# Optimization experiments

Measured on AMD Instinct MI355X. Metric: run time of the kernel, lower is better.

Reference implementation:

```python
import jax, jax.numpy as jnp
import numpy as np

B, L, S, LA, NA, E, D, H, NHID = 16, 256, 100, 48, 32, 64, 768, 12, 1024
W_IDX = S + 2
EPS = 1e-12


def setup_inputs() -> dict:
    rng = np.random.default_rng(0)
    key = jax.random.key(0)
    ks = jax.random.split(key, 8)
    idxs = np.zeros((B, W_IDX), dtype=np.int64)
    bert_lens = np.zeros((B,), dtype=np.int64)
    is_trig = np.zeros((B, S), dtype=np.float32)
    ent_map = np.zeros((B, S, E), dtype=np.float32)
    argw_mask = np.zeros((B, LA, 1), dtype=np.float32)
    for b in range(B):
        sb = int(rng.integers(60, S + 1))          # n first-subword tokens
        ab = int(rng.integers(8, LA + 1))          # n arg-role subwords
        sent_idx = np.sort(rng.choice(np.arange(1, 2 * sb + 1), size=sb, replace=False))
        sls = 2 * sb + 1                           # second-to-last [SEP] position
        last = sls + ab + 1                        # last [SEP] position
        idxs[b, :sb] = sent_idx
        idxs[b, sb] = sls
        idxs[b, sb + 1] = last
        bert_lens[b] = last + 1
        t0 = int(rng.integers(0, sb - 1))
        is_trig[b, t0:t0 + 2] = 1.0
        eb = int(rng.integers(16, E + 1))
        for e in range(eb):
            ent_map[b, int(rng.integers(0, sb)), e] = 1.0
        argw_mask[b, :ab, 0] = 1.0
    arg_w = np.asarray(jax.random.uniform(ks[0], (B, LA, NA), dtype=jnp.float32)) * argw_mask
    return {
        'all_embeddings': jax.random.normal(ks[1], (B, L, D), dtype=jnp.float32),
        'is_triggers': jnp.asarray(is_trig),
        'arg_weight_matrices': jnp.asarray(arg_w, dtype=jnp.float32),
        'entity_mapping': jnp.asarray(ent_map),
        'att0': jax.random.uniform(ks[2], (B, H, L, L), dtype=jnp.float32),
        'att1': jax.random.uniform(ks[3], (B, H, L, L), dtype=jnp.float32),
        'att2': jax.random.uniform(ks[4], (B, H, L, L), dtype=jnp.float32),
        'W_ta': jax.random.normal(ks[5], (3 * D, D), dtype=jnp.float32) * 0.02,
        'b_ta': jnp.zeros((D,), dtype=jnp.float32),
        'W1': jax.random.normal(ks[6], (6 * D, NHID), dtype=jnp.float32) * 0.02,
        'b1': jnp.zeros((NHID,), dtype=jnp.float32),
        'W2': jax.random.normal(ks[7], (NHID, 1), dtype=jnp.float32) * 0.02,
        'b2': jnp.zeros((1,), dtype=jnp.float32),
        'idxs_to_collect': jnp.asarray(idxs),
        'bert_sentence_lengths': jnp.asarray(bert_lens),
    }


def _l1_normalize(x, axis):
    # F.normalize(x, p=1, dim=axis)
    return x / jnp.clip(jnp.sum(jnp.abs(x), axis=axis, keepdims=True), EPS)


def reference(all_embeddings, is_triggers, arg_weight_matrices, entity_mapping,
              att0, att1, att2, W_ta, b_ta, W1, b1, W2, b2,
              idxs_to_collect, bert_sentence_lengths):
    idxs = idxs_to_collect
    valid = idxs > 0                                   # [B,W]
    n_valid = jnp.sum(valid, axis=1)                   # [B]
    j = jnp.arange(S)
    sent_valid = (j[None, :] < (n_valid - 2)[:, None]).astype(all_embeddings.dtype)  # [B,S]
    sent_idx = idxs[:, :S]
    # first-subword gather, zero-padded (get_fist_subword_embeddings)
    sent_emb = jnp.take_along_axis(all_embeddings, sent_idx[:, :, None], axis=1) * sent_valid[:, :, None]
    # arg-role segment: (second_last_sep+1) .. (bert_len-2), zero-padded to LA
    sls = jnp.take_along_axis(idxs, (n_valid - 2)[:, None], axis=1)[:, 0]   # [B]
    arg_pos = sls[:, None] + 1 + jnp.arange(LA)[None, :]                    # [B,LA]
    arg_valid = (arg_pos < (bert_sentence_lengths - 1)[:, None]).astype(all_embeddings.dtype)
    arg_emb0 = jnp.take_along_axis(all_embeddings, jnp.clip(arg_pos, 0, L - 1)[:, :, None], axis=1) * arg_valid[:, :, None]
    # entity aggregation + trigger mean pooling
    entity = jnp.einsum('bsd,bse->bed', sent_emb, entity_mapping)           # [B,E,D]
    trig = jnp.sum(sent_emb * is_triggers[:, :, None], axis=1) / jnp.sum(is_triggers, axis=1)[:, None]
    arg = jnp.einsum('bld,bla->bad', arg_emb0, arg_weight_matrices)         # [B,NA,D]
    # trigger-aware entity fusion
    trig_e = jnp.broadcast_to(trig[:, None, :], entity.shape)
    nonempty = (jnp.sum(jnp.abs(entity), axis=-1) > 0).astype(entity.dtype)
    ent_cat = jnp.concatenate([entity, trig_e, entity * trig_e], axis=-1)   # [B,E,3D]
    entity = (ent_cat @ W_ta + b_ta) * nonempty[:, :, None]
    # bidirectional token<->arg attention (L1-normalized)
    score = jnp.einsum('bed,bad->bea', entity, arg) / np.sqrt(D)            # [B,E,NA]
    t2a = _l1_normalize(score, 2)[..., None]
    a2t = _l1_normalize(score, 1)[..., None]
    token_argAwared = jnp.sum(arg[:, None] * t2a, axis=2)                   # [B,E,D]
    arg_tokenAwared = jnp.sum(entity[:, :, None] * a2t, axis=1)             # [B,NA,D]
    # select_hidden_att: head-mean, gather collected rows/cols, row-renormalize
    def sel_att(att):
        m = jnp.mean(att, axis=1)                                           # [B,L,L]
        r = jnp.take_along_axis(m, sent_idx[:, :, None], axis=1)            # [B,S,L]
        c = jnp.take_along_axis(r, sent_idx[:, None, :], axis=2)            # [B,S,S]
        c = c * sent_valid[:, :, None] * sent_valid[:, None, :]
        return c / jnp.clip(jnp.sum(c, axis=-1, keepdims=True), EPS)
    t2t = (sel_att(att0) + sel_att(att1) + sel_att(att2)) / 3.0             # [B,S,S]
    a_h2h_tok = t2t @ sent_emb                                              # [B,S,D]
    A_h2h = jnp.einsum('bse,bsd->bed', entity_mapping, a_h2h_tok)           # [B,E,D]
    H_ = jnp.einsum('bse,bsd->bed', entity_mapping, sent_emb)               # [B,E,D]
    a2a = jax.nn.softmax(arg @ jnp.swapaxes(arg, -1, -2), axis=-1)
    A_u2u = a2a @ arg                                                       # [B,NA,D]
    shp = (B, E, NA, D)
    latent = jnp.concatenate([
        jnp.broadcast_to(H_[:, :, None], shp),
        jnp.broadcast_to(arg[:, None], shp),
        jnp.broadcast_to(token_argAwared[:, :, None], shp),
        jnp.broadcast_to(A_h2h[:, :, None], shp),
        jnp.broadcast_to(arg_tokenAwared[:, None], shp),
        jnp.broadcast_to(A_u2u[:, None], shp),
    ], axis=-1)                                                             # [B,E,NA,6D]
    h = jax.nn.gelu(latent @ W1 + b1, approximate=False)
    out = (h @ W2 + b2)[..., 0]                                             # [B,E,NA]
    return out
```

## Files before the change

kernel.cpp:

```cpp
#include <hip/hip_runtime.h>
#include <math.h>

#define B_ 16
#define L_ 256
#define S_ 100
#define LA_ 48
#define NA_ 32
#define E_ 64
#define D_ 768
#define H_ 12
#define NHID_ 1024
#define WIDX_ 102
#define EPSF 1e-12f

typedef __attribute__((ext_vector_type(8))) short s16x8;
typedef __attribute__((ext_vector_type(4))) float f32x4;

__device__ __forceinline__ void split_bf16(float x, unsigned short& h, unsigned short& l) {
  unsigned u = __float_as_uint(x);
  unsigned hr = u + 0x7FFFu + ((u >> 16) & 1u);
  h = (unsigned short)(hr >> 16);
  float r = x - __uint_as_float(hr & 0xFFFF0000u);
  unsigned u2 = __float_as_uint(r);
  unsigned lr = u2 + 0x7FFFu + ((u2 >> 16) & 1u);
  l = (unsigned short)(lr >> 16);
}

__global__ void k_meta(const int* __restrict__ idxs, const int* __restrict__ blen,
                       int* __restrict__ meta) {
  int b = blockIdx.x, t = threadIdx.x;
  __shared__ int cnt;
  if (t == 0) cnt = 0;
  __syncthreads();
  if (t < WIDX_ && idxs[b * WIDX_ + t] > 0) atomicAdd(&cnt, 1);
  __syncthreads();
  if (t == 0) {
    int sb = cnt - 2;
    meta[b * 4 + 0] = sb;
    meta[b * 4 + 1] = idxs[b * WIDX_ + sb];
    meta[b * 4 + 2] = blen[b] - 1;
  }
}

__global__ void k_gather(const float* __restrict__ emb, const int* __restrict__ idxs,
                         const int* __restrict__ meta, float* __restrict__ sent_emb,
                         float* __restrict__ arg_emb) {
  int b = blockIdx.y, y = blockIdx.x, t = threadIdx.x;
  int sb = meta[b * 4 + 0], sls = meta[b * 4 + 1], last = meta[b * 4 + 2];
  if (y < S_) {
    int s = y;
    float* dst = sent_emb + ((size_t)b * S_ + s) * D_;
    if (s < sb) {
      const float* src = emb + ((size_t)b * L_ + idxs[b * WIDX_ + s]) * D_;
      for (int d = t; d < D_; d += 256) dst[d] = src[d];
    } else {
      for (int d = t; d < D_; d += 256) dst[d] = 0.f;
    }
  } else {
    int l = y - S_;
    int pos = sls + 1 + l;
    float* dst = arg_emb + ((size_t)b * LA_ + l) * D_;
    if (pos < last) {
      int p = pos > (L_ - 1) ? (L_ - 1) : pos;
      const float* src = emb + ((size_t)b * L_ + p) * D_;
      for (int d = t; d < D_; d += 256) dst[d] = src[d];
    } else {
      for (int d = t; d < D_; d += 256) dst[d] = 0.f;
    }
  }
}

__global__ void k_trig(const float* __restrict__ sent_emb, const float* __restrict__ is_trig,
                       float* __restrict__ trig) {
  int b = blockIdx.y;
  int d = blockIdx.x * 256 + threadIdx.x;
  float acc = 0.f, den = 0.f;
  for (int s = 0; s < S_; s++) {
    float w = is_trig[b * S_ + s];
    den += w;
    if (w != 0.f) acc += w * sent_emb[((size_t)b * S_ + s) * D_ + d];
  }
  trig[b * D_ + d] = acc / den;
}

__global__ __launch_bounds__(256) void k_entity0(const float* __restrict__ sent_emb,
                                                 const float* __restrict__ ent_map,
                                                 const float* __restrict__ trig,
                                                 unsigned short* __restrict__ e0h,
                                                 unsigned short* __restrict__ e0l,
                                                 unsigned short* __restrict__ e0th,
                                                 unsigned short* __restrict__ e0tl,
                                                 float* __restrict__ ne) {
  int b = blockIdx.y, e = blockIdx.x, t = threadIdx.x;
  float a0 = 0.f, a1 = 0.f, a2 = 0.f;
  for (int s = 0; s < S_; s++) {
    float w = ent_map[((size_t)b * S_ + s) * E_ + e];
    if (w != 0.f) {
      const float* r = sent_emb + ((size_t)b * S_ + s) * D_;
      a0 += w * r[t]; a1 += w * r[t + 256]; a2 += w * r[t + 512];
    }
  }
  size_t o = ((size_t)b * E_ + e) * D_;
  const float* tr = trig + b * D_;
  unsigned short h, lo;
  split_bf16(a0, h, lo); e0h[o + t] = h; e0l[o + t] = lo;
  split_bf16(a1, h, lo); e0h[o + t + 256] = h; e0l[o + t + 256] = lo;
  split_bf16(a2, h, lo); e0h[o + t + 512] = h; e0l[o + t + 512] = lo;
  split_bf16(a0 * tr[t], h, lo); e0th[o + t] = h; e0tl[o + t] = lo;
  split_bf16(a1 * tr[t + 256], h, lo); e0th[o + t + 256] = h; e0tl[o + t + 256] = lo;
  split_bf16(a2 * tr[t + 512], h, lo); e0th[o + t + 512] = h; e0tl[o + t + 512] = lo;
  __shared__ float red[256];
  red[t] = fabsf(a0) + fabsf(a1) + fabsf(a2);
  __syncthreads();
  for (int s2 = 128; s2 > 0; s2 >>= 1) {
    if (t < s2) red[t] += red[t + s2];
    __syncthreads();
  }
  if (t == 0) ne[b * E_ + e] = (red[0] > 0.f) ? 1.f : 0.f;
}

__global__ __launch_bounds__(256) void k_wsum(const float* __restrict__ Wm, int wstride, int sy,
                                              int sx, const float* __restrict__ Vm,
                                              float* __restrict__ Om,
                                              unsigned short* __restrict__ oh,
                                              unsigned short* __restrict__ ol, int Y) {
  int b = blockIdx.y, x = blockIdx.x, t = threadIdx.x;
  float a0 = 0.f, a1 = 0.f, a2 = 0.f;
  const float* wb = Wm + (size_t)b * wstride + (size_t)x * sx;
  const float* vb = Vm + (size_t)b * Y * D_;
  for (int y = 0; y < Y; y++) {
    float w = wb[(size_t)y * sy];
    if (w != 0.f) {
      const float* r = vb + (size_t)y * D_;
      a0 += w * r[t]; a1 += w * r[t + 256]; a2 += w * r[t + 512];
    }
  }
  size_t oidx = ((size_t)b * gridDim.x + x) * D_;
  if (Om) {
    Om[oidx + t] = a0; Om[oidx + t + 256] = a1; Om[oidx + t + 512] = a2;
  }
  if (oh) {
    unsigned short h, lo;
    split_bf16(a0, h, lo); oh[oidx + t] = h; ol[oidx + t] = lo;
    split_bf16(a1, h, lo); oh[oidx + t + 256] = h; ol[oidx + t + 256] = lo;
    split_bf16(a2, h, lo); oh[oidx + t + 512] = h; ol[oidx + t + 512] = lo;
  }
}

__global__ void k_tb(const float* __restrict__ trig, const float* __restrict__ W_ta,
                     const float* __restrict__ b_ta, float* __restrict__ tb) {
  int b = blockIdx.y;
  int d = blockIdx.x * 256 + threadIdx.x;
  float acc0 = b_ta[d], acc1 = 0.f, acc2 = 0.f, acc3 = 0.f;
  float acc4 = 0.f, acc5 = 0.f, acc6 = 0.f, acc7 = 0.f;
  const float* tr = trig + b * D_;
  const float* w = W_ta + (size_t)D_ * D_ + d;
  for (int k = 0; k < D_; k += 8) {
    acc0 += tr[k + 0] * w[(size_t)(k + 0) * D_];
    acc1 += tr[k + 1] * w[(size_t)(k + 1) * D_];
    acc2 += tr[k + 2] * w[(size_t)(k + 2) * D_];
    acc3 += tr[k + 3] * w[(size_t)(k + 3) * D_];
    acc4 += tr[k + 4] * w[(size_t)(k + 4) * D_];
    acc5 += tr[k + 5] * w[(size_t)(k + 5) * D_];
    acc6 += tr[k + 6] * w[(size_t)(k + 6) * D_];
    acc7 += tr[k + 7] * w[(size_t)(k + 7) * D_];
  }
  tb[b * D_ + d] = ((acc0 + acc1) + (acc2 + acc3)) + ((acc4 + acc5) + (acc6 + acc7));
}

__global__ __launch_bounds__(256) void k_cvtT(const float* __restrict__ src, int K, int N,
                                              unsigned short* __restrict__ th,
                                              unsigned short* __restrict__ tl) {
  __shared__ float tile[32][33];
  int k0 = blockIdx.x * 32, n0 = blockIdx.y * 32;
  int tr = threadIdx.x >> 3, c4 = (threadIdx.x & 7) * 4;
  float4 v = *(const float4*)(src + (size_t)(k0 + tr) * N + n0 + c4);
  tile[tr][c4] = v.x; tile[tr][c4 + 1] = v.y; tile[tr][c4 + 2] = v.z; tile[tr][c4 + 3] = v.w;
  __syncthreads();
  unsigned short h[4], l[4];
#pragma unroll
  for (int i = 0; i < 4; ++i) split_bf16(tile[c4 + i][tr], h[i], l[i]);
  size_t oo = (size_t)(n0 + tr) * K + k0 + c4;
  th[oo + 0] = h[0]; th[oo + 1] = h[1]; th[oo + 2] = h[2]; th[oo + 3] = h[3];
  tl[oo + 0] = l[0]; tl[oo + 1] = l[1]; tl[oo + 2] = l[2]; tl[oo + 3] = l[3];
}

__global__ __launch_bounds__(256) void k_mgemm(
    int phase,
    const unsigned short* __restrict__ e0h, const unsigned short* __restrict__ e0l,
    const unsigned short* __restrict__ e0th, const unsigned short* __restrict__ e0tl,
    const unsigned short* __restrict__ Ah2hh, const unsigned short* __restrict__ Ah2hl,
    const unsigned short* __restrict__ argmh, const unsigned short* __restrict__ argml,
    const unsigned short* __restrict__ Au2uh, const unsigned short* __restrict__ Au2ul,
    const unsigned short* __restrict__ entnh, const unsigned short* __restrict__ entnl,
    const unsigned short* __restrict__ WtaTh, const unsigned short* __restrict__ WtaTl,
    const unsigned short* __restrict__ W1Th, const unsigned short* __restrict__ W1Tl,
    float* __restrict__ Cpe, float* __restrict__ PeAp, float* __restrict__ PaAp,
    float* __restrict__ P2p, float* __restrict__ Q2p) {
  int z = blockIdx.z;
  const unsigned short *Ah_, *Al_, *Bh_, *Bl_;
  float* C;
  int bstride, mtiles, niter, N, akoff, bkoff;
  const size_t HPE = (size_t)B_ * E_ * NHID_;
  const size_t HPA = (size_t)B_ * NA_ * NHID_;
  if (phase == 0) {
    int job = z >> 1, kh = z & 1;
    if (job == 0) {
      Ah_ = kh ? e0th : e0h; Al_ = kh ? e0tl : e0l; Bh_ = WtaTh; Bl_ = WtaTl;
      bstride = 2304; akoff = 0; bkoff = kh ? 1536 : 0;
      C = Cpe + (size_t)kh * 1024 * 768; N = 768; mtiles = 16; niter = 24;
    } else if (job == 1) {
      Ah_ = kh ? Ah2hh : e0h; Al_ = kh ? Ah2hl : e0l; Bh_ = W1Th; Bl_ = W1Tl;
      bstride = 4608; akoff = 0; bkoff = kh ? 3 * 768 : 0;
      C = PeAp + kh * HPE; N = 1024; mtiles = 16; niter = 24;
    } else if (job == 2) {
      Ah_ = kh ? Au2uh : argmh; Al_ = kh ? Au2ul : argml; Bh_ = W1Th; Bl_ = W1Tl;
      bstride = 4608; akoff = 0; bkoff = kh ? 5 * 768 : 768;
      C = PaAp + kh * HPA; N = 1024; mtiles = 8; niter = 24;
    } else {
      Ah_ = argmh; Al_ = argml; Bh_ = W1Th; Bl_ = W1Tl;
      bstride = 4608; akoff = kh * 384; bkoff = 2 * 768 + kh * 384;
      C = P2p + kh * HPA; N = 1024; mtiles = 8; niter = 12;
    }
  } else {
    int kh = z;
    Ah_ = entnh; Al_ = entnl; Bh_ = W1Th; Bl_ = W1Tl;
    bstride = 4608; akoff = kh * 384; bkoff = 4 * 768 + kh * 384;
    C = Q2p + kh * HPE; N = 1024; mtiles = 16; niter = 12;
  }
  int bx = blockIdx.x, by = blockIdx.y;
  if (by >= mtiles || bx * 64 >= N) return;

  __shared__ unsigned short As[2][2][64][4][8];
  __shared__ unsigned short Bs[2][2][64][4][8];

  int tid = threadIdx.x;
  int srow = tid >> 2, sg = tid & 3;
  int wc = sg ^ ((srow >> 1) & 3);
  const unsigned short* aPh = Ah_ + (size_t)(by * 64 + srow) * 768 + akoff + sg * 8;
  const unsigned short* aPl = Al_ + (size_t)(by * 64 + srow) * 768 + akoff + sg * 8;
  const unsigned short* bPh = Bh_ + (size_t)(bx * 64 + srow) * bstride + bkoff + sg * 8;
  const unsigned short* bPl = Bl_ + (size_t)(bx * 64 + srow) * bstride + bkoff + sg * 8;

  int lane = tid & 63, wave = tid >> 6;
  int wm = wave >> 1, wn = wave & 1;
  int fg = lane >> 4, fr = lane & 15;
  int ar0 = wm * 32 + fr;
  int bc0 = wn * 32 + fr;
  int ca = fg ^ ((ar0 >> 1) & 3);
  int cb = fg ^ ((bc0 >> 1) & 3);

  f32x4 acc00 = {0.f, 0.f, 0.f, 0.f}, acc01 = {0.f, 0.f, 0.f, 0.f};
  f32x4 acc10 = {0.f, 0.f, 0.f, 0.f}, acc11 = {0.f, 0.f, 0.f, 0.f};

  s16x8 a0h = *(const s16x8*)(aPh + 0), a0l = *(const s16x8*)(aPl + 0);
  s16x8 b0h = *(const s16x8*)(bPh + 0), b0l = *(const s16x8*)(bPl + 0);
  s16x8 a1h = *(const s16x8*)(aPh + 32), a1l = *(const s16x8*)(aPl + 32);
  s16x8 b1h = *(const s16x8*)(bPh + 32), b1l = *(const s16x8*)(bPl + 32);

#define WRITE_LDS(buf, ah, al, bh, bl)              \
  {                                                 \
    *(s16x8*)&As[buf][0][srow][wc][0] = ah;         \
    *(s16x8*)&As[buf][1][srow][wc][0] = al;         \
    *(s16x8*)&Bs[buf][0][srow][wc][0] = bh;         \
    *(s16x8*)&Bs[buf][1][srow][wc][0] = bl;         \
  }
#define LOAD_SET(ah, al, bh, bl, t_)                \
  {                                                 \
    ah = *(const s16x8*)(aPh + (t_) * 32);          \
    al = *(const s16x8*)(aPl + (t_) * 32);          \
    bh = *(const s16x8*)(bPh + (t_) * 32);          \
    bl = *(const s16x8*)(bPl + (t_) * 32);          \
  }
#define READ_MFMA(buf)                                                          \
  {                                                                             \
    s16x8 xah0 = *(const s16x8*)&As[buf][0][ar0][ca][0];                        \
    s16x8 xah1 = *(const s16x8*)&As[buf][0][ar0 + 16][ca][0];                   \
    s16x8 xal0 = *(const s16x8*)&As[buf][1][ar0][ca][0];                        \
    s16x8 xal1 = *(const s16x8*)&As[buf][1][ar0 + 16][ca][0];                   \
    s16x8 xbh0 = *(const s16x8*)&Bs[buf][0][bc0][cb][0];                        \
    s16x8 xbh1 = *(const s16x8*)&Bs[buf][0][bc0 + 16][cb][0];                   \
    s16x8 xbl0 = *(const s16x8*)&Bs[buf][1][bc0][cb][0];                        \
    s16x8 xbl1 = *(const s16x8*)&Bs[buf][1][bc0 + 16][cb][0];                   \
    acc00 = __builtin_amdgcn_mfma_f32_16x16x32_bf16(xah0, xbh0, acc00, 0, 0, 0); \
    acc00 = __builtin_amdgcn_mfma_f32_16x16x32_bf16(xah0, xbl0, acc00, 0, 0, 0); \
    acc00 = __builtin_amdgcn_mfma_f32_16x16x32_bf16(xal0, xbh0, acc00, 0, 0, 0); \
    acc01 = __builtin_amdgcn_mfma_f32_16x16x32_bf16(xah0, xbh1, acc01, 0, 0, 0); \
    acc01 = __builtin_amdgcn_mfma_f32_16x16x32_bf16(xah0, xbl1, acc01, 0, 0, 0); \
    acc01 = __builtin_amdgcn_mfma_f32_16x16x32_bf16(xal0, xbh1, acc01, 0, 0, 0); \
    acc10 = __builtin_amdgcn_mfma_f32_16x16x32_bf16(xah1, xbh0, acc10, 0, 0, 0); \
    acc10 = __builtin_amdgcn_mfma_f32_16x16x32_bf16(xah1, xbl0, acc10, 0, 0, 0); \
    acc10 = __builtin_amdgcn_mfma_f32_16x16x32_bf16(xal1, xbh0, acc10, 0, 0, 0); \
    acc11 = __builtin_amdgcn_mfma_f32_16x16x32_bf16(xah1, xbh1, acc11, 0, 0, 0); \
    acc11 = __builtin_amdgcn_mfma_f32_16x16x32_bf16(xah1, xbl1, acc11, 0, 0, 0); \
    acc11 = __builtin_amdgcn_mfma_f32_16x16x32_bf16(xal1, xbh1, acc11, 0, 0, 0); \
  }

  WRITE_LDS(0, a0h, a0l, b0h, b0l);
  LOAD_SET(a0h, a0l, b0h, b0l, 2);
  __syncthreads();

  for (int it = 0; it < niter; it += 2) {
    if (it + 1 < niter) {
      WRITE_LDS(1, a1h, a1l, b1h, b1l);
      if (it + 3 < niter) LOAD_SET(a1h, a1l, b1h, b1l, it + 3);
    }
    READ_MFMA(0);
    __syncthreads();
    if (it + 2 < niter) {
      WRITE_LDS(0, a0h, a0l, b0h, b0l);
      if (it + 4 < niter) LOAD_SET(a0h, a0l, b0h, b0l, it + 4);
    }
    READ_MFMA(1);
    __syncthreads();
  }
#undef WRITE_LDS
#undef LOAD_SET
#undef READ_MFMA

  f32x4 accs[2][2] = {{acc00, acc01}, {acc10, acc11}};
  int colb = bx * 64 + wn * 32 + fr;
  int rowb = by * 64 + wm * 32 + fg * 4;
#pragma unroll
  for (int i = 0; i < 2; ++i) {
#pragma unroll
    for (int j = 0; j < 2; ++j) {
      int col = colb + j * 16;
#pragma unroll
      for (int r = 0; r < 4; ++r) {
        int row = rowb + i * 16 + r;
        C[(size_t)row * N + col] = accs[i][j][r];
      }
    }
  }
}

__global__ __launch_bounds__(256) void k_combE(const float* __restrict__ Cpe,
                                               const float* __restrict__ tb,
                                               const float* __restrict__ ne,
                                               float* __restrict__ entn,
                                               unsigned short* __restrict__ entnh,
                                               unsigned short* __restrict__ entnl) {
  int t = threadIdx.x;
  int r0 = blockIdx.x * 4;
  const size_t HH = (size_t)1024 * 768;
#pragma unroll
  for (int i = 0; i < 4; ++i) {
    int row = r0 + i;
    int b = row >> 6;
    float nev = ne[row];
#pragma unroll
    for (int j = 0; j < 3; ++j) {
      int col = t + j * 256;
      size_t o = (size_t)row * D_ + col;
      float v = (Cpe[o] + Cpe[HH + o] + tb[(size_t)b * D_ + col]) * nev;
      entn[o] = v;
      unsigned short hh, ll;
      split_bf16(v, hh, ll);
      entnh[o] = hh; entnl[o] = ll;
    }
  }
}

__global__ __launch_bounds__(256) void k_score(const float* __restrict__ entn,
                                               const float* __restrict__ argm,
                                               float* __restrict__ score) {
  int b = blockIdx.y, e = blockIdx.x, t = threadIdx.x;
  __shared__ float ent[D_];
  const float* er = entn + ((size_t)b * E_ + e) * D_;
  for (int d = t; d < D_; d += 256) ent[d] = er[d];
  __syncthreads();
  int wave = t >> 6, lane = t & 63;
  const float scale = 0.03608439182435161f;
  for (int a = wave; a < NA_; a += 4) {
    const float* ar = argm + ((size_t)b * NA_ + a) * D_;
    float p = 0.f;
#pragma unroll
    for (int i = 0; i < 12; i++) {
      int d = lane + 64 * i;
      p += ent[d] * ar[d];
    }
    for (int off = 32; off > 0; off >>= 1) p += __shfl_down(p, off);
    if (lane == 0) score[((size_t)b * E_ + e) * NA_ + a] = p * scale;
  }
}

__global__ void k_norm(const float* __restrict__ score, float* __restrict__ t2a,
                       float* __restrict__ a2t) {
  int b = blockIdx.x, t = threadIdx.x;
  __shared__ float s[E_ * NA_];
  __shared__ float rs[E_];
  __shared__ float cs[NA_];
  for (int i = t; i < E_ * NA_; i += 256) s[i] = score[(size_t)b * E_ * NA_ + i];
  __syncthreads();
  if (t < E_) {
    float sum = 0.f;
    for (int a = 0; a < NA_; a++) sum += fabsf(s[t * NA_ + a]);
    rs[t] = fmaxf(sum, EPSF);
  } else if (t >= 64 && t < 96) {
    int a = t - 64;
    float sum = 0.f;
    for (int e = 0; e < E_; e++) sum += fabsf(s[e * NA_ + a]);
    cs[a] = fmaxf(sum, EPSF);
  }
  __syncthreads();
  for (int i = t; i < E_ * NA_; i += 256) {
    int e = i >> 5, a = i & 31;
    float v = s[i];
    t2a[(size_t)b * E_ * NA_ + i] = v / rs[e];
    a2t[(size_t)b * E_ * NA_ + i] = v / cs[a];
  }
}

__global__ __launch_bounds__(256) void k_a2a(const float* __restrict__ argm,
                                             float* __restrict__ a2a) {
  int b = blockIdx.y, a = blockIdx.x, t = threadIdx.x;
  __shared__ float sA[D_];
  __shared__ float lg[NA_];
  const float* ar = argm + ((size_t)b * NA_ + a) * D_;
  for (int d = t; d < D_; d += 256) sA[d] = ar[d];
  __syncthreads();
  int wave = t >> 6, lane = t & 63;
  for (int a2 = wave; a2 < NA_; a2 += 4) {
    const float* br = argm + ((size_t)b * NA_ + a2) * D_;
    float p = 0.f;
#pragma unroll
    for (int i = 0; i < 12; i++) {
      int d = lane + 64 * i;
      p += sA[d] * br[d];
    }
    for (int off = 32; off > 0; off >>= 1) p += __shfl_down(p, off);
    if (lane == 0) lg[a2] = p;
  }
  __syncthreads();
  if (t < 64) {
    float v = (t < NA_) ? lg[t] : -INFINITY;
    float m = v;
    for (int mask = 16; mask > 0; mask >>= 1) m = fmaxf(m, __shfl_xor(m, mask));
    float ex = (t < NA_) ? expf(v - m) : 0.f;
    float sm = ex;
    for (int mask = 16; mask > 0; mask >>= 1) sm += __shfl_xor(sm, mask);
    if (t < NA_) a2a[((size_t)b * NA_ + a) * NA_ + t] = ex / sm;
  }
}

__global__ __launch_bounds__(128) void k_t2t(const float* __restrict__ att0,
                                             const float* __restrict__ att1,
                                             const float* __restrict__ att2,
                                             const int* __restrict__ idxs,
                                             const int* __restrict__ meta,
                                             float* __restrict__ t2t) {
  int b = blockIdx.y, s = blockIdx.x, t = threadIdx.x;
  int sb = meta[b * 4 + 0];
  float* out = t2t + ((size_t)b * S_ + s) * S_;
  if (s >= sb) {
    for (int j = t; j < S_; j += 128) out[j] = 0.f;
    return;
  }
  int Is = idxs[b * WIDX_ + s];
  int It = (t < S_) ? idxs[b * WIDX_ + t] : 0;
  __shared__ float row[256];
  __shared__ float red[128];
  const float* atts[3] = {att0, att1, att2};
  float accout = 0.f;
  for (int q = 0; q < 3; q++) {
    float r0 = 0.f, r1 = 0.f;
    const float* base = atts[q] + (((size_t)b * H_) * L_ + Is) * L_;
    for (int h = 0; h < H_; h++) {
      const float* rp = base + (size_t)h * L_ * L_;
      r0 += rp[t];
      r1 += rp[t + 128];
    }
    row[t] = r0;
    row[t + 128] = r1;
    __syncthreads();
    float v = (t < sb) ? row[It] * (1.f / 12.f) : 0.f;
    red[t] = v;
    __syncthreads();
    for (int s2 = 64; s2 > 0; s2 >>= 1) {
      if (t < s2) red[t] += red[t + s2];
      __syncthreads();
    }
    float rsum = red[0];
    __syncthreads();
    accout += v / fmaxf(rsum, EPSF) * (1.f / 3.f);
  }
  if (t < S_) out[t] = accout;
}

__global__ __launch_bounds__(256) void k_mix(const float* __restrict__ PeAp,
                                             const float* __restrict__ PaAp,
                                             const float* __restrict__ P2p,
                                             const float* __restrict__ Q2p,
                                             const float* __restrict__ t2a,
                                             const float* __restrict__ a2t,
                                             const float* __restrict__ b1,
                                             float* __restrict__ ps, float* __restrict__ qs) {
  int b = blockIdx.y, x = blockIdx.x, t = threadIdx.x;
  int n0 = t * 4;
  const size_t HPE = (size_t)B_ * E_ * NHID_;
  const size_t HPA = (size_t)B_ * NA_ * NHID_;
  __shared__ float w[E_];
  if (x < E_) {
    int e = x;
    size_t ro = ((size_t)b * E_ + e) * NHID_ + n0;
    float4 acc = *(const float4*)(PeAp + ro);
    float4 u1 = *(const float4*)(PeAp + HPE + ro);
    float4 bb = *(const float4*)(b1 + n0);
    acc.x += u1.x + bb.x; acc.y += u1.y + bb.y;
    acc.z += u1.z + bb.z; acc.w += u1.w + bb.w;
    if (t < NA_) w[t] = t2a[((size_t)b * E_ + e) * NA_ + t];
    __syncthreads();
    const float* pb = P2p + (size_t)b * NA_ * NHID_ + n0;
#pragma unroll 2
    for (int a = 0; a < NA_; a++) {
      float ww = w[a];
      float4 p0v = *(const float4*)(pb + (size_t)a * NHID_);
      float4 p1v = *(const float4*)(pb + HPA + (size_t)a * NHID_);
      acc.x += ww * (p0v.x + p1v.x); acc.y += ww * (p0v.y + p1v.y);
      acc.z += ww * (p0v.z + p1v.z); acc.w += ww * (p0v.w + p1v.w);
    }
    *(float4*)(ps + ro) = acc;
  } else {
    int a = x - E_;
    size_t ro = ((size_t)b * NA_ + a) * NHID_ + n0;
    float4 acc = *(const float4*)(PaAp + ro);
    float4 u1 = *(const float4*)(PaAp + HPA + ro);
    acc.x += u1.x; acc.y += u1.y; acc.z += u1.z; acc.w += u1.w;
    for (int i = t; i < E_; i += 256) w[i] = a2t[((size_t)b * E_ + i) * NA_ + a];
    __syncthreads();
    const float* qb = Q2p + (size_t)b * E_ * NHID_ + n0;
#pragma unroll 2
    for (int e = 0; e < E_; e++) {
      float ww = w[e];
      float4 q0v = *(const float4*)(qb + (size_t)e * NHID_);
      float4 q1v = *(const float4*)(qb + HPE + (size_t)e * NHID_);
      acc.x += ww * (q0v.x + q1v.x); acc.y += ww * (q0v.y + q1v.y);
      acc.z += ww * (q0v.z + q1v.z); acc.w += ww * (q0v.w + q1v.w);
    }
    *(float4*)(qs + ro) = acc;
  }
}

__global__ __launch_bounds__(256) void k_final(const float* __restrict__ ps,
                                               const float* __restrict__ qs,
                                               const float* __restrict__ W2,
                                               const float* __restrict__ b2,
                                               float* __restrict__ out) {
  int b = blockIdx.y, e = blockIdx.x, t = threadIdx.x;
  int wave = t >> 6, lane = t & 63;
  const float ks = 0.70710678118654752f;
  size_t po = ((size_t)b * E_ + e) * NHID_ + lane * 4;
  float4 p0 = *(const float4*)(ps + po);
  float4 p1 = *(const float4*)(ps + po + 256);
  float4 p2 = *(const float4*)(ps + po + 512);
  float4 p3 = *(const float4*)(ps + po + 768);
  const float* w2p = W2 + lane * 4;
  float4 w0 = *(const float4*)(w2p);
  float4 w1 = *(const float4*)(w2p + 256);
  float4 w2 = *(const float4*)(w2p + 512);
  float4 w3 = *(const float4*)(w2p + 768);
  __shared__ float outs[NA_];
#pragma unroll 2
  for (int a = wave; a < NA_; a += 4) {
    size_t qo = ((size_t)b * NA_ + a) * NHID_ + lane * 4;
    float4 q0 = *(const float4*)(qs + qo);
    float4 q1 = *(const float4*)(qs + qo + 256);
    float4 q2 = *(const float4*)(qs + qo + 512);
    float4 q3 = *(const float4*)(qs + qo + 768);
    float acc = 0.f;
#define GEL4(pp, qq, ww)                                          \
    {                                                             \
      float x0 = pp.x + qq.x, x1 = pp.y + qq.y;                   \
      float x2 = pp.z + qq.z, x3 = pp.w + qq.w;                   \
      float g0 = 0.5f * x0 * (1.f + erff(x0 * ks));               \
      float g1 = 0.5f * x1 * (1.f + erff(x1 * ks));               \
      float g2 = 0.5f * x2 * (1.f + erff(x2 * ks));               \
      float g3 = 0.5f * x3 * (1.f + erff(x3 * ks));               \
      acc += g0 * ww.x + g1 * ww.y + g2 * ww.z + g3 * ww.w;       \
    }
    GEL4(p0, q0, w0)
    GEL4(p1, q1, w1)
    GEL4(p2, q2, w2)
    GEL4(p3, q3, w3)
#undef GEL4
    acc += __shfl_xor(acc, 32);
    acc += __shfl_xor(acc, 16);
    acc += __shfl_xor(acc, 8);
    acc += __shfl_xor(acc, 4);
    acc += __shfl_xor(acc, 2);
    acc += __shfl_xor(acc, 1);
    if (lane == 0) outs[a] = acc;
  }
  __syncthreads();
  if (t < NA_) out[((size_t)b * E_ + e) * NA_ + t] = outs[t] + b2[0];
}

extern "C" void kernel_launch(void* const* d_in, const int* in_sizes, int n_in,
                              void* d_out, int out_size, void* d_ws, size_t ws_size,
                              hipStream_t stream) {
  const float* emb    = (const float*)d_in[0];
  const float* istrig = (const float*)d_in[1];
  const float* argw   = (const float*)d_in[2];
  const float* entmap = (const float*)d_in[3];
  const float* att0   = (const float*)d_in[4];
  const float* att1   = (const float*)d_in[5];
  const float* att2   = (const float*)d_in[6];
  const float* W_ta   = (const float*)d_in[7];
  const float* b_ta   = (const float*)d_in[8];
  const float* W1     = (const float*)d_in[9];
  const float* b1     = (const float*)d_in[10];
  const float* W2     = (const float*)d_in[11];
  const float* b2     = (const float*)d_in[12];
  const int*   idxs   = (const int*)d_in[13];
  const int*   blen   = (const int*)d_in[14];
  float* out = (float*)d_out;

  float* ws = (float*)d_ws;
  size_t o = 0;
  int* meta = (int*)ws; o += 256;
  float* sent_emb = ws + o; o += (size_t)B_ * S_ * D_;
  float* arg_emb  = ws + o; o += (size_t)B_ * LA_ * D_;
  float* trig     = ws + o; o += (size_t)B_ * D_;
  float* argm     = ws + o; o += (size_t)B_ * NA_ * D_;
  float* entn     = ws + o; o += (size_t)B_ * E_ * D_;
  float* tb       = ws + o; o += (size_t)B_ * D_;
  float* ne       = ws + o; o += (size_t)B_ * E_;
  float* score    = ws + o; o += (size_t)B_ * E_ * NA_;
  float* t2a      = ws + o; o += (size_t)B_ * E_ * NA_;
  float* a2t      = ws + o; o += (size_t)B_ * E_ * NA_;
  float* t2t      = ws + o; o += (size_t)B_ * S_ * S_;
  float* ah2h     = ws + o; o += (size_t)B_ * S_ * D_;
  float* a2a      = ws + o; o += (size_t)B_ * NA_ * NA_;
  float* Cpe      = ws + o; o += (size_t)2 * 1024 * 768;
  float* PeAp     = ws + o; o += (size_t)2 * B_ * E_ * NHID_;
  float* PaAp     = ws + o; o += (size_t)2 * B_ * NA_ * NHID_;
  float* P2p      = ws + o; o += (size_t)2 * B_ * NA_ * NHID_;
  float* Q2p      = ws + o; o += (size_t)2 * B_ * E_ * NHID_;
  float* ps = sent_emb;
  float* qs = arg_emb;

  o = (o + 3) & ~(size_t)3;
  unsigned short* us = (unsigned short*)(ws + o);
  size_t uo = 0;
  unsigned short* e0h   = us + uo; uo += (size_t)B_ * E_ * D_;
  unsigned short* e0l   = us + uo; uo += (size_t)B_ * E_ * D_;
  unsigned short* e0th  = us + uo; uo += (size_t)B_ * E_ * D_;
  unsigned short* e0tl  = us + uo; uo += (size_t)B_ * E_ * D_;
  unsigned short* Ah2hh = us + uo; uo += (size_t)B_ * E_ * D_;
  unsigned short* Ah2hl = us + uo; uo += (size_t)B_ * E_ * D_;
  unsigned short* argmh = us + uo; uo += (size_t)B_ * NA_ * D_;
  unsigned short* argml = us + uo; uo += (size_t)B_ * NA_ * D_;
  unsigned short* Au2uh = us + uo; uo += (size_t)B_ * NA_ * D_;
  unsigned short* Au2ul = us + uo; uo += (size_t)B_ * NA_ * D_;
  unsigned short* entnh = us + uo; uo += (size_t)B_ * E_ * D_;
  unsigned short* entnl = us + uo; uo += (size_t)B_ * E_ * D_;
  unsigned short* WtaTh = us + uo; uo += (size_t)2304 * 768;
  unsigned short* WtaTl = us + uo; uo += (size_t)2304 * 768;
  unsigned short* W1Th  = us + uo; uo += (size_t)4608 * 1024;
  unsigned short* W1Tl  = us + uo; uo += (size_t)4608 * 1024;

  k_meta<<<B_, 128, 0, stream>>>(idxs, blen, meta);
  k_cvtT<<<dim3(2304 / 32, 768 / 32), 256, 0, stream>>>(W_ta, 2304, 768, WtaTh, WtaTl);
  k_cvtT<<<dim3(4608 / 32, 1024 / 32), 256, 0, stream>>>(W1, 4608, 1024, W1Th, W1Tl);
  k_gather<<<dim3(S_ + LA_, B_), 256, 0, stream>>>(emb, idxs, meta, sent_emb, arg_emb);
  k_trig<<<dim3(3, B_), 256, 0, stream>>>(sent_emb, istrig, trig);
  k_entity0<<<dim3(E_, B_), 256, 0, stream>>>(sent_emb, entmap, trig, e0h, e0l, e0th, e0tl, ne);
  k_wsum<<<dim3(NA_, B_), 256, 0, stream>>>(argw, LA_ * NA_, NA_, 1, arg_emb, argm, argmh,
                                            argml, LA_);
  k_tb<<<dim3(3, B_), 256, 0, stream>>>(trig, W_ta, b_ta, tb);
  k_t2t<<<dim3(S_, B_), 128, 0, stream>>>(att0, att1, att2, idxs, meta, t2t);
  k_wsum<<<dim3(S_, B_), 256, 0, stream>>>(t2t, S_ * S_, 1, S_, sent_emb, ah2h, nullptr,
                                           nullptr, S_);
  k_wsum<<<dim3(E_, B_), 256, 0, stream>>>(entmap, S_ * E_, E_, 1, ah2h, nullptr, Ah2hh,
                                           Ah2hl, S_);
  k_a2a<<<dim3(NA_, B_), 256, 0, stream>>>(argm, a2a);
  k_wsum<<<dim3(NA_, B_), 256, 0, stream>>>(a2a, NA_ * NA_, 1, NA_, argm, nullptr, Au2uh,
                                            Au2ul, NA_);

  k_mgemm<<<dim3(16, 16, 8), 256, 0, stream>>>(0, e0h, e0l, e0th, e0tl, Ah2hh, Ah2hl, argmh,
                                               argml, Au2uh, Au2ul, entnh, entnl, WtaTh,
                                               WtaTl, W1Th, W1Tl, Cpe, PeAp, PaAp, P2p, Q2p);

  k_combE<<<dim3(B_ * E_ / 4), 256, 0, stream>>>(Cpe, tb, ne, entn, entnh, entnl);

  k_mgemm<<<dim3(16, 16, 2), 256, 0, stream>>>(1, e0h, e0l, e0th, e0tl, Ah2hh, Ah2hl, argmh,
                                               argml, Au2uh, Au2ul, entnh, entnl, WtaTh,
                                               WtaTl, W1Th, W1Tl, Cpe, PeAp, PaAp, P2p, Q2p);

  k_score<<<dim3(E_, B_), 256, 0, stream>>>(entn, argm, score);
  k_norm<<<B_, 256, 0, stream>>>(score, t2a, a2t);
  k_mix<<<dim3(E_ + NA_, B_), 256, 0, stream>>>(PeAp, PaAp, P2p, Q2p, t2a, a2t, b1, ps, qs);

  k_final<<<dim3(E_, B_), 256, 0, stream>>>(ps, qs, W2, b2, out);
}
```

Before: 510.9 us.

## Flatten multi-GEMM grid with XCD-aware mapping, drop split-K, fuse normalization into mix

```diff
diff --git a/kernel.cpp b/kernel.cpp
--- a/kernel.cpp
+++ b/kernel.cpp
@@ -196,40 +196,52 @@
     const unsigned short* __restrict__ WtaTh, const unsigned short* __restrict__ WtaTl,
     const unsigned short* __restrict__ W1Th, const unsigned short* __restrict__ W1Tl,
     float* __restrict__ Cpe, float* __restrict__ PeAp, float* __restrict__ PaAp,
-    float* __restrict__ P2p, float* __restrict__ Q2p) {
-  int z = blockIdx.z;
+    float* __restrict__ P2, float* __restrict__ Q2) {
+  const size_t HPE = (size_t)B_ * E_ * NHID_;
+  const size_t HPA = (size_t)B_ * NA_ * NHID_;
+  const size_t HH = (size_t)1024 * 768;
+  int flat = blockIdx.x;
+  int xcd = flat & 7;
+  int i = flat >> 3;
+  int by8 = i & 7;
+  int colIdx = i >> 3;
+  int job, bx, byTop = 0;
+  if (phase == 0) {
+    int gc = xcd * 20 + colIdx;
+    if (gc < 24)       { job = 0; int r = gc;       bx = r >> 1; byTop = (r & 1) << 3; }
+    else if (gc < 48)  { job = 1; int r = gc - 24;  bx = r >> 1; byTop = (r & 1) << 3; }
+    else if (gc < 80)  { job = 2; int r = gc - 48;  bx = r >> 1; byTop = (r & 1) << 3; }
+    else if (gc < 112) { job = 3; int r = gc - 80;  bx = r >> 1; byTop = (r & 1) << 3; }
+    else if (gc < 128) { job = 4; bx = gc - 112; }
+    else if (gc < 144) { job = 5; bx = gc - 128; }
+    else               { job = 6; bx = gc - 144; }
+  } else {
+    int gc = xcd * 4 + colIdx;
+    job = 7; bx = gc >> 1; byTop = (gc & 1) << 3;
+  }
+  int by = byTop + by8;
+
   const unsigned short *Ah_, *Al_, *Bh_, *Bl_;
   float* C;
-  int bstride, mtiles, niter, N, akoff, bkoff;
-  const size_t HPE = (size_t)B_ * E_ * NHID_;
-  const size_t HPA = (size_t)B_ * NA_ * NHID_;
-  if (phase == 0) {
-    int job = z >> 1, kh = z & 1;
-    if (job == 0) {
-      Ah_ = kh ? e0th : e0h; Al_ = kh ? e0tl : e0l; Bh_ = WtaTh; Bl_ = WtaTl;
-      bstride = 2304; akoff = 0; bkoff = kh ? 1536 : 0;
-      C = Cpe + (size_t)kh * 1024 * 768; N = 768; mtiles = 16; niter = 24;
-    } else if (job == 1) {
-      Ah_ = kh ? Ah2hh : e0h; Al_ = kh ? Ah2hl : e0l; Bh_ = W1Th; Bl_ = W1Tl;
-      bstride = 4608; akoff = 0; bkoff = kh ? 3 * 768 : 0;
-      C = PeAp + kh * HPE; N = 1024; mtiles = 16; niter = 24;
-    } else if (job == 2) {
-      Ah_ = kh ? Au2uh : argmh; Al_ = kh ? Au2ul : argml; Bh_ = W1Th; Bl_ = W1Tl;
-      bstride = 4608; akoff = 0; bkoff = kh ? 5 * 768 : 768;
-      C = PaAp + kh * HPA; N = 1024; mtiles = 8; niter = 24;
-    } else {
-      Ah_ = argmh; Al_ = argml; Bh_ = W1Th; Bl_ = W1Tl;
-      bstride = 4608; akoff = kh * 384; bkoff = 2 * 768 + kh * 384;
-      C = P2p + kh * HPA; N = 1024; mtiles = 8; niter = 12;
-    }
-  } else {
-    int kh = z;
-    Ah_ = entnh; Al_ = entnl; Bh_ = W1Th; Bl_ = W1Tl;
-    bstride = 4608; akoff = kh * 384; bkoff = 4 * 768 + kh * 384;
-    C = Q2p + kh * HPE; N = 1024; mtiles = 16; niter = 12;
-  }
-  int bx = blockIdx.x, by = blockIdx.y;
-  if (by >= mtiles || bx * 64 >= N) return;
+  int bstride, N, bkoff;
+  switch (job) {
+    case 0: Ah_ = e0h;   Al_ = e0l;   Bh_ = WtaTh; Bl_ = WtaTl; bstride = 2304;
+            bkoff = 0;        C = Cpe;        N = 768;  break;
+    case 1: Ah_ = e0th;  Al_ = e0tl;  Bh_ = WtaTh; Bl_ = WtaTl; bstride = 2304;
+            bkoff = 1536;     C = Cpe + HH;   N = 768;  break;
+    case 2: Ah_ = e0h;   Al_ = e0l;   Bh_ = W1Th;  Bl_ = W1Tl;  bstride = 4608;
+            bkoff = 0;        C = PeAp;       N = 1024; break;
+    case 3: Ah_ = Ah2hh; Al_ = Ah2hl; Bh_ = W1Th;  Bl_ = W1Tl;  bstride = 4608;
+            bkoff = 3 * 768;  C = PeAp + HPE; N = 1024; break;
+    case 4: Ah_ = argmh; Al_ = argml; Bh_ = W1Th;  Bl_ = W1Tl;  bstride = 4608;
+            bkoff = 768;      C = PaAp;       N = 1024; break;
+    case 5: Ah_ = Au2uh; Al_ = Au2ul; Bh_ = W1Th;  Bl_ = W1Tl;  bstride = 4608;
+            bkoff = 5 * 768;  C = PaAp + HPA; N = 1024; break;
+    case 6: Ah_ = argmh; Al_ = argml; Bh_ = W1Th;  Bl_ = W1Tl;  bstride = 4608;
+            bkoff = 2 * 768;  C = P2;         N = 1024; break;
+    default: Ah_ = entnh; Al_ = entnl; Bh_ = W1Th; Bl_ = W1Tl;  bstride = 4608;
+            bkoff = 4 * 768;  C = Q2;         N = 1024; break;
+  }
 
   __shared__ unsigned short As[2][2][64][4][8];
   __shared__ unsigned short Bs[2][2][64][4][8];
@@ -237,8 +249,8 @@
   int tid = threadIdx.x;
   int srow = tid >> 2, sg = tid & 3;
   int wc = sg ^ ((srow >> 1) & 3);
-  const unsigned short* aPh = Ah_ + (size_t)(by * 64 + srow) * 768 + akoff + sg * 8;
-  const unsigned short* aPl = Al_ + (size_t)(by * 64 + srow) * 768 + akoff + sg * 8;
+  const unsigned short* aPh = Ah_ + (size_t)(by * 64 + srow) * 768 + sg * 8;
+  const unsigned short* aPl = Al_ + (size_t)(by * 64 + srow) * 768 + sg * 8;
   const unsigned short* bPh = Bh_ + (size_t)(bx * 64 + srow) * bstride + bkoff + sg * 8;
   const unsigned short* bPl = Bl_ + (size_t)(bx * 64 + srow) * bstride + bkoff + sg * 8;
 
@@ -253,6 +265,7 @@
   f32x4 acc00 = {0.f, 0.f, 0.f, 0.f}, acc01 = {0.f, 0.f, 0.f, 0.f};
   f32x4 acc10 = {0.f, 0.f, 0.f, 0.f}, acc11 = {0.f, 0.f, 0.f, 0.f};
 
+  const int niter = 24;
   s16x8 a0h = *(const s16x8*)(aPh + 0), a0l = *(const s16x8*)(aPl + 0);
   s16x8 b0h = *(const s16x8*)(bPh + 0), b0l = *(const s16x8*)(bPl + 0);
   s16x8 a1h = *(const s16x8*)(aPh + 32), a1l = *(const s16x8*)(aPl + 32);
@@ -322,14 +335,14 @@
   int colb = bx * 64 + wn * 32 + fr;
   int rowb = by * 64 + wm * 32 + fg * 4;
 #pragma unroll
-  for (int i = 0; i < 2; ++i) {
+  for (int i2 = 0; i2 < 2; ++i2) {
 #pragma unroll
     for (int j = 0; j < 2; ++j) {
       int col = colb + j * 16;
 #pragma unroll
       for (int r = 0; r < 4; ++r) {
-        int row = rowb + i * 16 + r;
-        C[(size_t)row * N + col] = accs[i][j][r];
+        int row = rowb + i2 * 16 + r;
+        C[(size_t)row * N + col] = accs[i2][j][r];
       }
     }
   }
@@ -382,33 +395,6 @@
     }
     for (int off = 32; off > 0; off >>= 1) p += __shfl_down(p, off);
     if (lane == 0) score[((size_t)b * E_ + e) * NA_ + a] = p * scale;
-  }
-}
-
-__global__ void k_norm(const float* __restrict__ score, float* __restrict__ t2a,
-                       float* __restrict__ a2t) {
-  int b = blockIdx.x, t = threadIdx.x;
-  __shared__ float s[E_ * NA_];
-  __shared__ float rs[E_];
-  __shared__ float cs[NA_];
-  for (int i = t; i < E_ * NA_; i += 256) s[i] = score[(size_t)b * E_ * NA_ + i];
-  __syncthreads();
-  if (t < E_) {
-    float sum = 0.f;
-    for (int a = 0; a < NA_; a++) sum += fabsf(s[t * NA_ + a]);
-    rs[t] = fmaxf(sum, EPSF);
-  } else if (t >= 64 && t < 96) {
-    int a = t - 64;
-    float sum = 0.f;
-    for (int e = 0; e < E_; e++) sum += fabsf(s[e * NA_ + a]);
-    cs[a] = fmaxf(sum, EPSF);
-  }
-  __syncthreads();
-  for (int i = t; i < E_ * NA_; i += 256) {
-    int e = i >> 5, a = i & 31;
-    float v = s[i];
-    t2a[(size_t)b * E_ * NA_ + i] = v / rs[e];
-    a2t[(size_t)b * E_ * NA_ + i] = v / cs[a];
   }
 }
 
@@ -490,17 +476,16 @@
 
 __global__ __launch_bounds__(256) void k_mix(const float* __restrict__ PeAp,
                                              const float* __restrict__ PaAp,
-                                             const float* __restrict__ P2p,
-                                             const float* __restrict__ Q2p,
-                                             const float* __restrict__ t2a,
-                                             const float* __restrict__ a2t,
+                                             const float* __restrict__ P2,
+                                             const float* __restrict__ Q2,
+                                             const float* __restrict__ score,
                                              const float* __restrict__ b1,
                                              float* __restrict__ ps, float* __restrict__ qs) {
   int b = blockIdx.y, x = blockIdx.x, t = threadIdx.x;
   int n0 = t * 4;
   const size_t HPE = (size_t)B_ * E_ * NHID_;
   const size_t HPA = (size_t)B_ * NA_ * NHID_;
-  __shared__ float w[E_];
+  __shared__ float sc[E_];
   if (x < E_) {
     int e = x;
     size_t ro = ((size_t)b * E_ + e) * NHID_ + n0;
@@ -509,16 +494,17 @@
     float4 bb = *(const float4*)(b1 + n0);
     acc.x += u1.x + bb.x; acc.y += u1.y + bb.y;
     acc.z += u1.z + bb.z; acc.w += u1.w + bb.w;
-    if (t < NA_) w[t] = t2a[((size_t)b * E_ + e) * NA_ + t];
-    __syncthreads();
-    const float* pb = P2p + (size_t)b * NA_ * NHID_ + n0;
+    if (t < NA_) sc[t] = score[((size_t)b * E_ + e) * NA_ + t];
+    __syncthreads();
+    float rs = 0.f;
+    for (int a = 0; a < NA_; a++) rs += fabsf(sc[a]);
+    rs = fmaxf(rs, EPSF);
+    const float* pb = P2 + (size_t)b * NA_ * NHID_ + n0;
 #pragma unroll 2
     for (int a = 0; a < NA_; a++) {
-      float ww = w[a];
-      float4 p0v = *(const float4*)(pb + (size_t)a * NHID_);
-      float4 p1v = *(const float4*)(pb + HPA + (size_t)a * NHID_);
-      acc.x += ww * (p0v.x + p1v.x); acc.y += ww * (p0v.y + p1v.y);
-      acc.z += ww * (p0v.z + p1v.z); acc.w += ww * (p0v.w + p1v.w);
+      float ww = sc[a] / rs;
+      float4 p = *(const float4*)(pb + (size_t)a * NHID_);
+      acc.x += ww * p.x; acc.y += ww * p.y; acc.z += ww * p.z; acc.w += ww * p.w;
     }
     *(float4*)(ps + ro) = acc;
   } else {
@@ -527,16 +513,17 @@
     float4 acc = *(const float4*)(PaAp + ro);
     float4 u1 = *(const float4*)(PaAp + HPA + ro);
     acc.x += u1.x; acc.y += u1.y; acc.z += u1.z; acc.w += u1.w;
-    for (int i = t; i < E_; i += 256) w[i] = a2t[((size_t)b * E_ + i) * NA_ + a];
-    __syncthreads();
-    const float* qb = Q2p + (size_t)b * E_ * NHID_ + n0;
+    if (t < E_) sc[t] = score[((size_t)b * E_ + t) * NA_ + a];
+    __syncthreads();
+    float cs = 0.f;
+    for (int e = 0; e < E_; e++) cs += fabsf(sc[e]);
+    cs = fmaxf(cs, EPSF);
+    const float* qb = Q2 + (size_t)b * E_ * NHID_ + n0;
 #pragma unroll 2
     for (int e = 0; e < E_; e++) {
-      float ww = w[e];
-      float4 q0v = *(const float4*)(qb + (size_t)e * NHID_);
-      float4 q1v = *(const float4*)(qb + HPE + (size_t)e * NHID_);
-      acc.x += ww * (q0v.x + q1v.x); acc.y += ww * (q0v.y + q1v.y);
-      acc.z += ww * (q0v.z + q1v.z); acc.w += ww * (q0v.w + q1v.w);
+      float ww = sc[e] / cs;
+      float4 q = *(const float4*)(qb + (size_t)e * NHID_);
+      acc.x += ww * q.x; acc.y += ww * q.y; acc.z += ww * q.z; acc.w += ww * q.w;
     }
     *(float4*)(qs + ro) = acc;
   }
@@ -627,16 +614,14 @@
   float* tb       = ws + o; o += (size_t)B_ * D_;
   float* ne       = ws + o; o += (size_t)B_ * E_;
   float* score    = ws + o; o += (size_t)B_ * E_ * NA_;
-  float* t2a      = ws + o; o += (size_t)B_ * E_ * NA_;
-  float* a2t      = ws + o; o += (size_t)B_ * E_ * NA_;
   float* t2t      = ws + o; o += (size_t)B_ * S_ * S_;
   float* ah2h     = ws + o; o += (size_t)B_ * S_ * D_;
   float* a2a      = ws + o; o += (size_t)B_ * NA_ * NA_;
   float* Cpe      = ws + o; o += (size_t)2 * 1024 * 768;
   float* PeAp     = ws + o; o += (size_t)2 * B_ * E_ * NHID_;
   float* PaAp     = ws + o; o += (size_t)2 * B_ * NA_ * NHID_;
-  float* P2p      = ws + o; o += (size_t)2 * B_ * NA_ * NHID_;
-  float* Q2p      = ws + o; o += (size_t)2 * B_ * E_ * NHID_;
+  float* P2       = ws + o; o += (size_t)B_ * NA_ * NHID_;
+  float* Q2       = ws + o; o += (size_t)B_ * E_ * NHID_;
   float* ps = sent_emb;
   float* qs = arg_emb;
 
@@ -678,19 +663,18 @@
   k_wsum<<<dim3(NA_, B_), 256, 0, stream>>>(a2a, NA_ * NA_, 1, NA_, argm, nullptr, Au2uh,
                                             Au2ul, NA_);
 
-  k_mgemm<<<dim3(16, 16, 8), 256, 0, stream>>>(0, e0h, e0l, e0th, e0tl, Ah2hh, Ah2hl, argmh,
-                                               argml, Au2uh, Au2ul, entnh, entnl, WtaTh,
-                                               WtaTl, W1Th, W1Tl, Cpe, PeAp, PaAp, P2p, Q2p);
+  k_mgemm<<<dim3(1280), 256, 0, stream>>>(0, e0h, e0l, e0th, e0tl, Ah2hh, Ah2hl, argmh,
+                                          argml, Au2uh, Au2ul, entnh, entnl, WtaTh, WtaTl,
+                                          W1Th, W1Tl, Cpe, PeAp, PaAp, P2, Q2);
 
   k_combE<<<dim3(B_ * E_ / 4), 256, 0, stream>>>(Cpe, tb, ne, entn, entnh, entnl);
 
-  k_mgemm<<<dim3(16, 16, 2), 256, 0, stream>>>(1, e0h, e0l, e0th, e0tl, Ah2hh, Ah2hl, argmh,
-                                               argml, Au2uh, Au2ul, entnh, entnl, WtaTh,
-                                               WtaTl, W1Th, W1Tl, Cpe, PeAp, PaAp, P2p, Q2p);
+  k_mgemm<<<dim3(256), 256, 0, stream>>>(1, e0h, e0l, e0th, e0tl, Ah2hh, Ah2hl, argmh,
+                                         argml, Au2uh, Au2ul, entnh, entnl, WtaTh, WtaTl,
+                                         W1Th, W1Tl, Cpe, PeAp, PaAp, P2, Q2);
 
   k_score<<<dim3(E_, B_), 256, 0, stream>>>(entn, argm, score);
-  k_norm<<<B_, 256, 0, stream>>>(score, t2a, a2t);
-  k_mix<<<dim3(E_ + NA_, B_), 256, 0, stream>>>(PeAp, PaAp, P2p, Q2p, t2a, a2t, b1, ps, qs);
+  k_mix<<<dim3(E_ + NA_, B_), 256, 0, stream>>>(PeAp, PaAp, P2, Q2, score, b1, ps, qs);
 
   k_final<<<dim3(E_, B_), 256, 0, stream>>>(ps, qs, W2, b2, out);
 }
```

Result: faster. 491.0 us (-3.9%).
